# Performance work log

Hardware: AMD Instinct MI355X
Metric: run time of the kernel (lower is better)

The kernel has to match this reference:

```python
import jax, jax.numpy as jnp
import numpy as np

N_EMBD = 1024
N_HEAD = 16
DIM_HEAD = N_EMBD // N_HEAD
SCALE = DIM_HEAD ** (-0.5)  # source divides by this (i.e. multiplies scores by sqrt(dim_head))


def setup_inputs() -> dict:
    key = jax.random.key(0)
    k1, k2, k3, k4, k5 = jax.random.split(key, 5)
    B, Tq, Tkv = 2, 2048, 2048
    x_q = jax.random.normal(k1, (B, Tq, N_EMBD), dtype=jnp.float32)
    x_kv = jax.random.normal(k2, (B, Tkv, N_EMBD), dtype=jnp.float32)
    s = 0.02
    W_q = jax.random.normal(k3, (N_EMBD, N_EMBD), dtype=jnp.float32) * s
    W_kv = jax.random.normal(k4, (N_EMBD, 2 * N_EMBD), dtype=jnp.float32) * s
    W_proj = jax.random.normal(k5, (N_EMBD, N_EMBD), dtype=jnp.float32) * s
    return {"x_q": x_q, "x_kv": x_kv, "W_q": W_q, "W_kv": W_kv, "W_proj": W_proj}


def reference(x_q, x_kv, W_q, W_kv, W_proj):
    B, Tq, C = x_q.shape
    Tkv = x_kv.shape[1]
    q = x_q @ W_q                      # [B, Tq, C]
    kv = x_kv @ W_kv                   # [B, Tkv, 2C]
    k, v = jnp.split(kv, 2, axis=2)
    # [B, H, T, Dh]
    q = q.reshape(B, Tq, N_HEAD, DIM_HEAD).transpose(0, 2, 1, 3)
    k = k.reshape(B, Tkv, N_HEAD, DIM_HEAD).transpose(0, 2, 1, 3)
    v = v.reshape(B, Tkv, N_HEAD, DIM_HEAD).transpose(0, 2, 1, 3)
    # Faithful to source: scores = q@k^T / scale  (== * sqrt(dim_head))
    attn = jnp.einsum('bhqd,bhkd->bhqk', q, k) / SCALE
    attn = jax.nn.softmax(attn, axis=-1)
    y = jnp.einsum('bhqk,bhkd->bhqd', attn, v)
    y = y.transpose(0, 2, 1, 3).reshape(B, Tq, C)
    return y @ W_proj
```

## Files before the change

### kernel.cpp

```cpp
#include <hip/hip_runtime.h>
#include <cstddef>

typedef _Float16 f16;
typedef _Float16 f16x8 __attribute__((ext_vector_type(8)));
typedef _Float16 f16x4 __attribute__((ext_vector_type(4)));
typedef _Float16 f16x2 __attribute__((ext_vector_type(2)));
typedef float f32x4 __attribute__((ext_vector_type(4)));
typedef float f32x16 __attribute__((ext_vector_type(16)));
typedef unsigned int u32;

__device__ inline float exp2_fast(float x) {
  float r;
  asm("v_exp_f32 %0, %1" : "=v"(r) : "v"(x));
  return r;
}

__device__ inline int pk2(float x, float y) {
  return __builtin_bit_cast(int, __builtin_amdgcn_cvt_pkrtz(x, y));
}

__device__ inline f16x2 pk2h(float x, float y) {
  return __builtin_bit_cast(f16x2, __builtin_amdgcn_cvt_pkrtz(x, y));
}

__device__ inline void permlane32_swap(int& a, int& b) {
  asm volatile("v_permlane32_swap_b32 %0, %1" : "+v"(a), "+v"(b));
}

__device__ __forceinline__ void gload16(const f16* g, f16* l) {
  __builtin_amdgcn_global_load_lds(
      (const __attribute__((address_space(1))) void*)g,
      (__attribute__((address_space(3))) void*)l, 16, 0, 0);
}

__global__ __launch_bounds__(256) void prep(
    const float* __restrict__ xq, const float* __restrict__ xkv,
    f16* __restrict__ oq, f16* __restrict__ okv,
    const float* __restrict__ Wq, const float* __restrict__ Wkv,
    const float* __restrict__ Wp, f16* __restrict__ Wqt,
    f16* __restrict__ Wkvt, f16* __restrict__ Wpt) {
  __shared__ float t[32][33];
  int bid = blockIdx.x;
  if (bid < 8192) {
    const float* in = (bid < 4096) ? xq : xkv;
    f16* out = (bid < 4096) ? oq : okv;
    int i = ((bid & 4095) * 256 + threadIdx.x) * 4;
    float4 v = *(const float4*)&in[i];
    f16x4 h;
    h[0] = (f16)v.x; h[1] = (f16)v.y; h[2] = (f16)v.z; h[3] = (f16)v.w;
    *(f16x4*)&out[i] = h;
  } else {
    int zz = bid - 8192;
    int bx = zz & 31, by = (zz >> 5) & 31, z = zz >> 10;
    const float* in;
    f16* out;
    int N = 1024, extra = 0;
    if (z == 0) { in = Wq; out = Wqt; }
    else if (z == 3) { in = Wp; out = Wpt; }
    else { in = Wkv; out = Wkvt; N = 2048; extra = (z - 1) * 1024; }
    int tx = threadIdx.x % 32, ty = threadIdx.x / 32;
    int n0 = bx * 32 + extra, k0 = by * 32;
#pragma unroll
    for (int i = 0; i < 32; i += 8)
      t[ty + i][tx] = in[(size_t)(k0 + ty + i) * N + n0 + tx];
    __syncthreads();
#pragma unroll
    for (int i = 0; i < 32; i += 8)
      out[(size_t)(n0 + ty + i) * 1024 + k0 + tx] = (f16)t[tx][ty + i];
  }
}

template <int BN, typename CT>
__device__ __forceinline__ void gemm_body(
    const f16* __restrict__ A, const f16* __restrict__ Bt, CT* __restrict__ C,
    int bid, int M, int N, int K, float scale, f16* As, f16* Bs) {
  constexpr int NT = BN / 32;
  const int nb = N / BN;
  const int nwg = (M / 128) * nb;
  const int sbid = (bid & 7) * (nwg >> 3) + (bid >> 3);
  const int m0 = (sbid / nb) * 128;
  const int n0 = (sbid % nb) * BN;
  const int tid = threadIdx.x;
  const int w = tid >> 6, lane = tid & 63;
  const int l16 = lane & 15, quad = lane >> 4;
  const int wrow = (w >> 1) * 64, wcol = (w & 1) * (BN / 2);
  const int lrow = lane >> 3, lcol = (lane & 7) * 8;

  f32x4 acc[4][NT] = {};

  for (int k0 = 0; k0 < K; k0 += 64) {
#pragma unroll
    for (int i = 0; i < 4; i++) {
      const int r = w * 32 + i * 8;
      gload16(&A[(size_t)(m0 + r + lrow) * K + k0 + lcol], &As[r * 64]);
    }
#pragma unroll
    for (int i = 0; i < NT; i++) {
      const int r = w * (BN / 4) + i * 8;
      gload16(&Bt[(size_t)(n0 + r + lrow) * K + k0 + lcol], &Bs[r * 64]);
    }
    __syncthreads();

    f16x8 bf[NT][2];
#pragma unroll
    for (int nt = 0; nt < NT; nt++) {
      const int row = wcol + nt * 16 + l16;
#pragma unroll
      for (int s = 0; s < 2; s++)
        bf[nt][s] = *(const f16x8*)&Bs[row * 64 + s * 32 + quad * 8];
    }
#pragma unroll
    for (int mt = 0; mt < 4; mt++) {
      const int row = wrow + mt * 16 + l16;
      f16x8 af0 = *(const f16x8*)&As[row * 64 + quad * 8];
      f16x8 af1 = *(const f16x8*)&As[row * 64 + 32 + quad * 8];
#pragma unroll
      for (int nt = 0; nt < NT; nt++) {
        acc[mt][nt] = __builtin_amdgcn_mfma_f32_16x16x32_f16(af0, bf[nt][0], acc[mt][nt], 0, 0, 0);
        acc[mt][nt] = __builtin_amdgcn_mfma_f32_16x16x32_f16(af1, bf[nt][1], acc[mt][nt], 0, 0, 0);
      }
    }
    __syncthreads();
  }

#pragma unroll
  for (int mt = 0; mt < 4; mt++)
#pragma unroll
    for (int nt = 0; nt < NT; nt++)
#pragma unroll
      for (int r = 0; r < 4; r++) {
        int row = m0 + wrow + mt * 16 + quad * 4 + r;
        int col = n0 + wcol + nt * 16 + l16;
        C[(size_t)row * N + col] = (CT)(acc[mt][nt][r] * scale);
      }
}

__global__ __launch_bounds__(256, 3) void qkv_gemm(
    const f16* __restrict__ Xq, const f16* __restrict__ Wqt, f16* __restrict__ Qh,
    const f16* __restrict__ Xkv, const f16* __restrict__ Wkvt, f16* __restrict__ KVh,
    float sc_q) {
  __shared__ f16 As[128 * 64];
  __shared__ f16 Bs[128 * 64];
  if (blockIdx.x < 256)
    gemm_body<128, f16>(Xq, Wqt, Qh, blockIdx.x, 4096, 1024, 1024, sc_q, As, Bs);
  else
    gemm_body<128, f16>(Xkv, Wkvt, KVh, blockIdx.x - 256, 4096, 2048, 1024, 1.0f, As, Bs);
}

template <int BN, typename CT>
__global__ __launch_bounds__(256, 2) void gemm_lds(
    const f16* __restrict__ A, const f16* __restrict__ Bt, CT* __restrict__ C,
    int M, int N, int K, float scale) {
  __shared__ f16 As[128 * 64];
  __shared__ f16 Bs[BN * 64];
  gemm_body<BN, CT>(A, Bt, C, blockIdx.x, M, N, K, scale, As, Bs);
}

__global__ __launch_bounds__(512, 4) void attn_kernel(
    const f16* __restrict__ Qh, const f16* __restrict__ KVh, f16* __restrict__ Yh) {
  __shared__ f16 smem[18432];

  const int bid = blockIdx.x;
  const int hb = bid & 31;
  const int qt = bid >> 5;
  const int h = hb >> 1, b = hb & 1;
  const int tid = threadIdx.x;
  const int w = tid >> 6, lane = tid & 63;
  const int l31 = lane & 31, e = lane >> 5;
  const int qw = w & 3, half = w >> 2;
  const int tl = tid & 255;

  f16* Ks = smem + half * (2 * 64 * 72);
  f16* Vt = Ks + 64 * 72;

  const size_t qrow0 = (size_t)b * 2048 + (size_t)qt * 128;
  const size_t kvrow0 = (size_t)b * 2048 + (size_t)half * 1024;

  f16x8 qf[4];
#pragma unroll
  for (int ks = 0; ks < 4; ks++)
    qf[ks] = *(const f16x8*)&Qh[(qrow0 + qw * 32 + l31) * 1024 + h * 64 + ks * 16 + e * 8];

  float m_run = -1e30f, l_run = 0.0f;
  f32x16 o_acc[2] = {};

  const int ksr = tl >> 2, ksc = (tl & 3) << 4;
  const int vkv0 = (tl >> 3) * 2;
  const int vd0 = (tl & 7) * 8;
  const int vcol = ((((vkv0 >> 3) ^ (tl & 7)) << 3) | (vkv0 & 7));

  f16x8 kr0, kr1, vr0, vr1;
  {
    const f16* kb = &KVh[(kvrow0 + ksr) * 2048 + h * 64 + ksc];
    kr0 = *(const f16x8*)kb;
    kr1 = *(const f16x8*)(kb + 8);
    const f16* vb = &KVh[(kvrow0 + vkv0) * 2048 + 1024 + h * 64 + vd0];
    vr0 = *(const f16x8*)vb;
    vr1 = *(const f16x8*)(vb + 2048);
  }

  for (int t = 0; t < 16; t++) {
    *(f16x8*)&Ks[ksr * 72 + ksc] = kr0;
    *(f16x8*)&Ks[ksr * 72 + ksc + 8] = kr1;
#pragma unroll
    for (int j = 0; j < 8; j++) {
      f16x2 p; p[0] = vr0[j]; p[1] = vr1[j];
      *(f16x2*)&Vt[(vd0 + j) * 72 + vcol] = p;
    }
    __syncthreads();

    if (t + 1 < 16) {
      const f16* kb = &KVh[(kvrow0 + (t + 1) * 64 + ksr) * 2048 + h * 64 + ksc];
      kr0 = *(const f16x8*)kb;
      kr1 = *(const f16x8*)(kb + 8);
      const f16* vb = &KVh[(kvrow0 + (t + 1) * 64 + vkv0) * 2048 + 1024 + h * 64 + vd0];
      vr0 = *(const f16x8*)vb;
      vr1 = *(const f16x8*)(vb + 2048);
    }

    f32x16 sacc[2] = {};
#pragma unroll
    for (int kvt = 0; kvt < 2; kvt++)
#pragma unroll
      for (int ks = 0; ks < 4; ks++) {
        f16x8 a = *(const f16x8*)&Ks[(kvt * 32 + l31) * 72 + ks * 16 + e * 8];
        sacc[kvt] = __builtin_amdgcn_mfma_f32_32x32x16_f16(a, qf[ks], sacc[kvt], 0, 0, 0);
      }

    float mxa[4];
#pragma unroll
    for (int j = 0; j < 4; j++) {
      float a = fmaxf(fmaxf(sacc[0][j], sacc[0][j + 4]),
                      fmaxf(sacc[0][j + 8], sacc[0][j + 12]));
      float bb = fmaxf(fmaxf(sacc[1][j], sacc[1][j + 4]),
                       fmaxf(sacc[1][j + 8], sacc[1][j + 12]));
      mxa[j] = fmaxf(a, bb);
    }
    float mx = fmaxf(fmaxf(mxa[0], mxa[1]), fmaxf(mxa[2], mxa[3]));
    mx = fmaxf(mx, __shfl_xor(mx, 32, 64));

    if (!__all(mx <= m_run + 8.0f)) {
      float mnew = fmaxf(m_run, mx);
      float alpha = exp2_fast(m_run - mnew);
      m_run = mnew;
      l_run *= alpha;
#pragma unroll
      for (int r = 0; r < 16; r++) { o_acc[0][r] *= alpha; o_acc[1][r] *= alpha; }
    }

    float ss0 = 0.0f, ss1 = 0.0f, ss2 = 0.0f, ss3 = 0.0f;
#pragma unroll
    for (int kvt = 0; kvt < 2; kvt++)
#pragma unroll
      for (int r = 0; r < 16; r += 4) {
        float p0 = exp2_fast(sacc[kvt][r + 0] - m_run);
        float p1 = exp2_fast(sacc[kvt][r + 1] - m_run);
        float p2 = exp2_fast(sacc[kvt][r + 2] - m_run);
        float p3 = exp2_fast(sacc[kvt][r + 3] - m_run);
        sacc[kvt][r + 0] = p0; sacc[kvt][r + 1] = p1;
        sacc[kvt][r + 2] = p2; sacc[kvt][r + 3] = p3;
        ss0 += p0; ss1 += p1; ss2 += p2; ss3 += p3;
      }
    float ssum = (ss0 + ss1) + (ss2 + ss3);
    ssum += __shfl_xor(ssum, 32, 64);
    l_run += ssum;

    f16x8 pf[4];
#pragma unroll
    for (int kvt = 0; kvt < 2; kvt++)
#pragma unroll
      for (int hf = 0; hf < 2; hf++) {
        const int h8 = hf * 8;
        int a0 = pk2(sacc[kvt][h8 + 0], sacc[kvt][h8 + 1]);
        int b0 = pk2(sacc[kvt][h8 + 4], sacc[kvt][h8 + 5]);
        int a1 = pk2(sacc[kvt][h8 + 2], sacc[kvt][h8 + 3]);
        int b1 = pk2(sacc[kvt][h8 + 6], sacc[kvt][h8 + 7]);
        permlane32_swap(a0, b0);
        permlane32_swap(a1, b1);
        union { int i[4]; f16x8 v; } u;
        u.i[0] = a0; u.i[1] = a1; u.i[2] = b0; u.i[3] = b1;
        pf[kvt * 2 + hf] = u.v;
      }

#pragma unroll
    for (int dt = 0; dt < 2; dt++) {
      const int d = dt * 32 + l31;
      const int dx = d >> 3;
#pragma unroll
      for (int ks = 0; ks < 4; ks++) {
        f16x8 va = *(const f16x8*)&Vt[d * 72 + (((ks * 2 + e) ^ dx) << 3)];
        o_acc[dt] = __builtin_amdgcn_mfma_f32_32x32x16_f16(va, pf[ks], o_acc[dt], 0, 0, 0);
      }
    }
    __syncthreads();
  }

  float* Om = (float*)smem;
  float* ML = (float*)smem + 4 * 32 * 68;
  if (half == 1) {
#pragma unroll
    for (int dt = 0; dt < 2; dt++)
#pragma unroll
      for (int r2 = 0; r2 < 4; r2++) {
        f32x4 vv;
        vv[0] = o_acc[dt][r2 * 4 + 0];
        vv[1] = o_acc[dt][r2 * 4 + 1];
        vv[2] = o_acc[dt][r2 * 4 + 2];
        vv[3] = o_acc[dt][r2 * 4 + 3];
        *(f32x4*)&Om[(qw * 32 + l31) * 68 + dt * 32 + r2 * 8 + e * 4] = vv;
      }
    ML[qw * 64 + l31] = m_run;
    ML[qw * 64 + 32 + l31] = l_run;
  }
  __syncthreads();
  float linv = 0.0f;
  if (half == 0) {
    float m1 = ML[qw * 64 + l31], l1 = ML[qw * 64 + 32 + l31];
    float mm = fmaxf(m_run, m1);
    float a0 = exp2_fast(m_run - mm), a1 = exp2_fast(m1 - mm);
    linv = 1.0f / (l_run * a0 + l1 * a1);
#pragma unroll
    for (int dt = 0; dt < 2; dt++)
#pragma unroll
      for (int r2 = 0; r2 < 4; r2++) {
        f32x4 o1 = *(const f32x4*)&Om[(qw * 32 + l31) * 68 + dt * 32 + r2 * 8 + e * 4];
#pragma unroll
        for (int j = 0; j < 4; j++)
          o_acc[dt][r2 * 4 + j] = o_acc[dt][r2 * 4 + j] * a0 + o1[j] * a1;
      }
  }
  __syncthreads();

  if (half == 0) {
    f16* Of = smem + qw * 32 * 72;
#pragma unroll
    for (int dt = 0; dt < 2; dt++)
#pragma unroll
      for (int r2 = 0; r2 < 4; r2++) {
        f16x2 h0 = pk2h(o_acc[dt][r2 * 4 + 0] * linv, o_acc[dt][r2 * 4 + 1] * linv);
        f16x2 h1 = pk2h(o_acc[dt][r2 * 4 + 2] * linv, o_acc[dt][r2 * 4 + 3] * linv);
        f16x4 hh; hh[0] = h0[0]; hh[1] = h0[1]; hh[2] = h1[0]; hh[3] = h1[1];
        *(f16x4*)&Of[l31 * 72 + dt * 32 + r2 * 8 + e * 4] = hh;
      }
    const int qq = lane >> 1, dh = (lane & 1) * 32;
#pragma unroll
    for (int j = 0; j < 4; j++) {
      f16x8 v = *(const f16x8*)&Of[qq * 72 + dh + j * 8];
      *(f16x8*)&Yh[(qrow0 + qw * 32 + qq) * 1024 + h * 64 + dh + j * 8] = v;
    }
  }
}

extern "C" void kernel_launch(void* const* d_in, const int* in_sizes, int n_in,
                              void* d_out, int out_size, void* d_ws, size_t ws_size,
                              hipStream_t stream) {
  const float* x_q  = (const float*)d_in[0];
  const float* x_kv = (const float*)d_in[1];
  const float* W_q  = (const float*)d_in[2];
  const float* W_kv = (const float*)d_in[3];
  const float* W_p  = (const float*)d_in[4];
  float* out = (float*)d_out;

  f16* Wq_t  = (f16*)d_ws;
  f16* Wkv_t = Wq_t  + (size_t)1024 * 1024;
  f16* Wp_t  = Wkv_t + (size_t)2048 * 1024;
  f16* Qh    = Wp_t  + (size_t)1024 * 1024;
  f16* KVh   = Qh    + (size_t)4096 * 1024;
  f16* Yh    = KVh   + (size_t)4096 * 2048;
  f16* Xq_h  = Yh;
  f16* Xkv_h = Yh    + (size_t)4096 * 1024;

  prep<<<12288, 256, 0, stream>>>(x_q, x_kv, Xq_h, Xkv_h,
                                  W_q, W_kv, W_p, Wq_t, Wkv_t, Wp_t);

  const float SC = 11.5415603f;
  qkv_gemm<<<768, 256, 0, stream>>>(Xq_h, Wq_t, Qh, Xkv_h, Wkv_t, KVh, SC);

  attn_kernel<<<512, 512, 0, stream>>>(Qh, KVh, Yh);

  gemm_lds<64, float><<<512, 256, 0, stream>>>(Yh, Wp_t, out, 4096, 1024, 1024, 1.0f);
}
```

Measured before the change: 203.5 us.

## Double-buffer GEMM LDS tiles and XOR-swizzle layout to avoid bank conflicts

Result: no change. 203.1 us (-0.2%).

```diff
diff --git a/kernel.cpp b/kernel.cpp
--- a/kernel.cpp
+++ b/kernel.cpp
@@ -75,6 +75,8 @@
     const f16* __restrict__ A, const f16* __restrict__ Bt, CT* __restrict__ C,
     int bid, int M, int N, int K, float scale, f16* As, f16* Bs) {
   constexpr int NT = BN / 32;
+  constexpr int ASZ = 128 * 64;
+  constexpr int BSZ = BN * 64;
   const int nb = N / BN;
   const int nwg = (M / 128) * nb;
   const int sbid = (bid & 7) * (nwg >> 3) + (bid >> 3);
@@ -84,22 +86,34 @@
   const int w = tid >> 6, lane = tid & 63;
   const int l16 = lane & 15, quad = lane >> 4;
   const int wrow = (w >> 1) * 64, wcol = (w & 1) * (BN / 2);
-  const int lrow = lane >> 3, lcol = (lane & 7) * 8;
+  const int lrow = lane >> 3;
+  const int lcs = (((lane & 7) ^ (lane >> 3)) & 7) * 8;
 
   f32x4 acc[4][NT] = {};
 
+#define STAGE_TILE(bp, kk)                                                   \
+  {                                                                          \
+    _Pragma("unroll") for (int i = 0; i < 4; i++) {                          \
+      const int r = w * 32 + i * 8;                                          \
+      gload16(&A[(size_t)(m0 + r + lrow) * K + (kk) + lcs],                  \
+              &As[(bp) * ASZ + r * 64]);                                     \
+    }                                                                        \
+    _Pragma("unroll") for (int i = 0; i < NT; i++) {                         \
+      const int r = w * (BN / 4) + i * 8;                                    \
+      gload16(&Bt[(size_t)(n0 + r + lrow) * K + (kk) + lcs],                 \
+              &Bs[(bp) * BSZ + r * 64]);                                     \
+    }                                                                        \
+  }
+
+  STAGE_TILE(0, 0);
+  __syncthreads();
+
+  int buf = 0;
   for (int k0 = 0; k0 < K; k0 += 64) {
-#pragma unroll
-    for (int i = 0; i < 4; i++) {
-      const int r = w * 32 + i * 8;
-      gload16(&A[(size_t)(m0 + r + lrow) * K + k0 + lcol], &As[r * 64]);
-    }
-#pragma unroll
-    for (int i = 0; i < NT; i++) {
-      const int r = w * (BN / 4) + i * 8;
-      gload16(&Bt[(size_t)(n0 + r + lrow) * K + k0 + lcol], &Bs[r * 64]);
-    }
-    __syncthreads();
+    if (k0 + 64 < K) STAGE_TILE(buf ^ 1, k0 + 64);
+
+    const f16* Asb = &As[buf * ASZ];
+    const f16* Bsb = &Bs[buf * BSZ];
 
     f16x8 bf[NT][2];
 #pragma unroll
@@ -107,13 +121,13 @@
       const int row = wcol + nt * 16 + l16;
 #pragma unroll
       for (int s = 0; s < 2; s++)
-        bf[nt][s] = *(const f16x8*)&Bs[row * 64 + s * 32 + quad * 8];
+        bf[nt][s] = *(const f16x8*)&Bsb[row * 64 + (((s * 4 + quad) ^ (row & 7)) << 3)];
     }
 #pragma unroll
     for (int mt = 0; mt < 4; mt++) {
       const int row = wrow + mt * 16 + l16;
-      f16x8 af0 = *(const f16x8*)&As[row * 64 + quad * 8];
-      f16x8 af1 = *(const f16x8*)&As[row * 64 + 32 + quad * 8];
+      f16x8 af0 = *(const f16x8*)&Asb[row * 64 + ((quad ^ (row & 7)) << 3)];
+      f16x8 af1 = *(const f16x8*)&Asb[row * 64 + (((4 + quad) ^ (row & 7)) << 3)];
 #pragma unroll
       for (int nt = 0; nt < NT; nt++) {
         acc[mt][nt] = __builtin_amdgcn_mfma_f32_16x16x32_f16(af0, bf[nt][0], acc[mt][nt], 0, 0, 0);
@@ -121,7 +135,9 @@
       }
     }
     __syncthreads();
-  }
+    buf ^= 1;
+  }
+#undef STAGE_TILE
 
 #pragma unroll
   for (int mt = 0; mt < 4; mt++)
@@ -135,12 +151,12 @@
       }
 }
 
-__global__ __launch_bounds__(256, 3) void qkv_gemm(
+__global__ __launch_bounds__(256, 2) void qkv_gemm(
     const f16* __restrict__ Xq, const f16* __restrict__ Wqt, f16* __restrict__ Qh,
     const f16* __restrict__ Xkv, const f16* __restrict__ Wkvt, f16* __restrict__ KVh,
     float sc_q) {
-  __shared__ f16 As[128 * 64];
-  __shared__ f16 Bs[128 * 64];
+  __shared__ f16 As[2 * 128 * 64];
+  __shared__ f16 Bs[2 * 128 * 64];
   if (blockIdx.x < 256)
     gemm_body<128, f16>(Xq, Wqt, Qh, blockIdx.x, 4096, 1024, 1024, sc_q, As, Bs);
   else
@@ -148,11 +164,11 @@
 }
 
 template <int BN, typename CT>
-__global__ __launch_bounds__(256, 2) void gemm_lds(
+__global__ __launch_bounds__(256, 3) void gemm_lds(
     const f16* __restrict__ A, const f16* __restrict__ Bt, CT* __restrict__ C,
     int M, int N, int K, float scale) {
-  __shared__ f16 As[128 * 64];
-  __shared__ f16 Bs[BN * 64];
+  __shared__ f16 As[2 * 128 * 64];
+  __shared__ f16 Bs[2 * BN * 64];
   gemm_body<BN, CT>(A, Bt, C, blockIdx.x, M, N, K, scale, As, Bs);
 }
 
```
